# Kernel optimization log

Measured on AMD Instinct MI355X. Metric: run time of the kernel, lower is better.

Reference implementation:

```python
import jax, jax.numpy as jnp
import numpy as np

# Mamba2 config derived from __init__ defaults
D_MODEL, D_STATE, D_CONV, EXPAND, HEADDIM = 768, 16, 4, 2, 64
D_INNER = EXPAND * D_MODEL                      # 1536
NHEADS = D_INNER // HEADDIM                     # 24
NGROUPS = 1
CONV_DIM = D_INNER + 2 * NGROUPS * D_STATE      # 1568
D_IN_PROJ = 2 * D_INNER + 2 * NGROUPS * D_STATE + NHEADS  # 3128
EPS = 1e-5


def setup_inputs() -> dict:
    key = jax.random.key(0)
    ks = jax.random.split(key, 8)
    B, L = 2, 4096
    x = jax.random.normal(ks[0], (B, L, D_MODEL), jnp.float32)
    s_in = 1.0 / np.sqrt(D_MODEL)
    s_out = 1.0 / np.sqrt(D_INNER)
    W_in = jax.random.uniform(ks[1], (D_IN_PROJ, D_MODEL), jnp.float32, -s_in, s_in)
    W_out = jax.random.uniform(ks[2], (D_MODEL, D_INNER), jnp.float32, -s_out, s_out)
    conv_w = jax.random.uniform(ks[3], (CONV_DIM, D_CONV), jnp.float32, -0.5, 0.5)
    conv_b = jax.random.uniform(ks[4], (CONV_DIM,), jnp.float32, -0.5, 0.5)
    # dt init in [1e-3, 0.1] (log-uniform), stored as inverse-softplus bias
    dt = jnp.exp(jax.random.uniform(ks[5], (NHEADS,), jnp.float32) * (np.log(0.1) - np.log(1e-3)) + np.log(1e-3))
    dt_bias = dt + jnp.log(-jnp.expm1(-dt))
    A_log = jnp.log(jax.random.uniform(ks[6], (NHEADS,), jnp.float32, 1.0, 16.0))
    D = jnp.ones((NHEADS,), jnp.float32)
    ln_w = jnp.ones((D_MODEL,), jnp.float32)
    ln_b = jnp.zeros((D_MODEL,), jnp.float32)
    gate_norm_w = jnp.ones((D_INNER,), jnp.float32)
    return dict(x=x, ln_w=ln_w, ln_b=ln_b, W_in=W_in, conv_w=conv_w, conv_b=conv_b,
                dt_bias=dt_bias, A_log=A_log, D=D, gate_norm_w=gate_norm_w, W_out=W_out)


def _layernorm(x, w, b):
    mu = x.mean(-1, keepdims=True)
    var = ((x - mu) ** 2).mean(-1, keepdims=True)
    return (x - mu) * jax.lax.rsqrt(var + EPS) * w + b


def _silu(x):
    return x * jax.nn.sigmoid(x)


def _mamba_block(x, ln_w, ln_b, W_in, conv_w, conv_b, dt_bias, A_log, D, gate_norm_w, W_out):
    Bsz, L, _ = x.shape
    u = _layernorm(x, ln_w, ln_b)
    zxbcdt = jnp.einsum('bld,ed->ble', u, W_in)                 # (b,l,3128)
    z = zxbcdt[..., :D_INNER]
    xBC = zxbcdt[..., D_INNER:D_INNER + CONV_DIM]
    dt = jax.nn.softplus(zxbcdt[..., -NHEADS:] + dt_bias)       # (b,l,h)
    # causal depthwise conv (width D_CONV) + SiLU
    xp = jnp.pad(xBC, ((0, 0), (D_CONV - 1, 0), (0, 0)))
    acc = xp[:, 0:L, :] * conv_w[:, 0]
    for i in range(1, D_CONV):
        acc = acc + xp[:, i:i + L, :] * conv_w[:, i]
    xBC = _silu(acc + conv_b)
    xs = xBC[..., :D_INNER].reshape(Bsz, L, NHEADS, HEADDIM)    # (b,l,h,p)
    Bm = xBC[..., D_INNER:D_INNER + D_STATE]                    # (b,l,n) ngroups=1
    Cm = xBC[..., D_INNER + D_STATE:]                           # (b,l,n)
    A = -jnp.exp(A_log)                                         # (h,)
    dA = jnp.exp(dt * A)                                        # (b,l,h)
    # selective scan: h_t = dA_t * h_{t-1} + dt_t * (x_t outer B_t)
    def step(h, inp):
        dA_t, dt_t, B_t, C_t, x_t = inp                          # (b,h),(b,h),(b,n),(b,n),(b,h,p)
        h = dA_t[..., None, None] * h + jnp.einsum('bh,bn,bhp->bhpn', dt_t, B_t, x_t)
        y = jnp.einsum('bhpn,bn->bhp', h, C_t)
        return h, y
    h0 = jnp.zeros((Bsz, NHEADS, HEADDIM, D_STATE), x.dtype)
    _, ys = jax.lax.scan(step, h0, (dA.transpose(1, 0, 2), dt.transpose(1, 0, 2),
                                    Bm.transpose(1, 0, 2), Cm.transpose(1, 0, 2),
                                    xs.transpose(1, 0, 2, 3)))
    y = ys.transpose(1, 0, 2, 3) + D[:, None] * xs               # (b,l,h,p) skip term
    y = y.reshape(Bsz, L, D_INNER)
    # gated RMSNorm: norm(y * silu(z)) * weight
    g = y * _silu(z)
    g = g * jax.lax.rsqrt((g * g).mean(-1, keepdims=True) + EPS) * gate_norm_w
    out = jnp.einsum('ble,de->bld', g, W_out)
    return x + out


def reference(x, ln_w, ln_b, W_in, conv_w, conv_b, dt_bias, A_log, D, gate_norm_w, W_out):
    return _mamba_block(x, ln_w, ln_b, W_in, conv_w, conv_b, dt_bias, A_log, D, gate_norm_w, W_out)
```

## Files before the change

kernel.cpp:

```cpp
#include <hip/hip_runtime.h>
#include <hip/hip_bf16.h>
#include <stdint.h>

#define SEQ      4096
#define BATCH    2
#define NTOK     (BATCH*SEQ)
#define DMODEL   768
#define DINNER   1536
#define NHEADS   24
#define HEADDIM  64
#define DSTATE   16
#define NPAD     3200
#define EPSV     1e-5f
#define CHUNK    64
#define NCHUNK   (SEQ/CHUNK)
#define SUB      32
#define LNBLK    2048

typedef __bf16 bf16x8 __attribute__((ext_vector_type(8)));
typedef float  floatx4 __attribute__((ext_vector_type(4)));

__device__ __forceinline__ unsigned short f2bf(float f) {
    union { float f; uint32_t u; } v; v.f = f;
    uint32_t u = v.u;
    uint32_t r = (u + 0x7fffu + ((u >> 16) & 1u)) >> 16;
    return (unsigned short)r;
}

__device__ __forceinline__ float bf2f(unsigned short h) {
    union { uint32_t u; float f; } v; v.u = (uint32_t)h << 16;
    return v.f;
}

__device__ __forceinline__ float bfl(uint32_t u) {
    union { uint32_t u; float f; } v; v.u = u << 16; return v.f;
}
__device__ __forceinline__ float bfh(uint32_t u) {
    union { uint32_t u; float f; } v; v.u = u & 0xffff0000u; return v.f;
}
__device__ __forceinline__ uint32_t packbf(float lo, float hi) {
    return (uint32_t)f2bf(lo) | ((uint32_t)f2bf(hi) << 16);
}

__device__ __forceinline__ float siluf(float x) { return x / (1.f + __expf(-x)); }

__device__ __forceinline__ void async_cp16(const void* g, void* l) {
    __builtin_amdgcn_global_load_lds(
        (const __attribute__((address_space(1))) void*)g,
        (__attribute__((address_space(3))) void*)l,
        16, 0, 0);
}

__global__ __launch_bounds__(256) void prep_kernel(
    const float* __restrict__ x, const float* __restrict__ lnw, const float* __restrict__ lnb,
    unsigned short* __restrict__ u16,
    const float* __restrict__ Win, const float* __restrict__ Wout,
    const float* __restrict__ gw,
    unsigned short* __restrict__ win16, unsigned short* __restrict__ wout16)
{
    if (blockIdx.x < LNBLK) {
        int wave = threadIdx.x >> 6, lane = threadIdx.x & 63;
        int token = blockIdx.x * 4 + wave;
        const float* row = x + (size_t)token * DMODEL;
        float4 v[3];
        float s = 0.f, ss = 0.f;
#pragma unroll
        for (int j = 0; j < 3; ++j) {
            v[j] = *(const float4*)(row + lane*4 + j*256);
            s  += v[j].x + v[j].y + v[j].z + v[j].w;
            ss += v[j].x*v[j].x + v[j].y*v[j].y + v[j].z*v[j].z + v[j].w*v[j].w;
        }
#pragma unroll
        for (int o = 32; o > 0; o >>= 1) { s += __shfl_xor(s, o, 64); ss += __shfl_xor(ss, o, 64); }
        float mean = s * (1.f/768.f);
        float var  = ss * (1.f/768.f) - mean*mean;
        float rstd = rsqrtf(var + EPSV);
        unsigned short* brow = u16 + (size_t)token * DMODEL;
#pragma unroll
        for (int j = 0; j < 3; ++j) {
            int cidx = lane*4 + j*256;
            float4 w4 = *(const float4*)(lnw + cidx);
            float4 b4 = *(const float4*)(lnb + cidx);
            float a0 = (v[j].x - mean)*rstd*w4.x + b4.x;
            float a1 = (v[j].y - mean)*rstd*w4.y + b4.y;
            float a2 = (v[j].z - mean)*rstd*w4.z + b4.z;
            float a3 = (v[j].w - mean)*rstd*w4.w + b4.w;
            ushort4 p; p.x = f2bf(a0); p.y = f2bf(a1); p.z = f2bf(a2); p.w = f2bf(a3);
            *(ushort4*)(brow + cidx) = p;
        }
    } else {
        int e = ((blockIdx.x - LNBLK) * 256 + threadIdx.x) * 4;
        const int n1 = NPAD * DMODEL;
        if (e < n1) {
            int r = e / DMODEL;
            ushort4 p = {0, 0, 0, 0};
            if (r < 3128) {
                float4 v = *(const float4*)(Win + e);
                p.x = f2bf(v.x); p.y = f2bf(v.y); p.z = f2bf(v.z); p.w = f2bf(v.w);
            }
            *(ushort4*)(win16 + e) = p;
        } else {
            int e2 = e - n1;
            if (e2 < DMODEL * DINNER) {
                int row = e2 / DINNER;
                int col = e2 - row * DINNER;
                float4 v = *(const float4*)(Wout + e2);
                float4 w = *(const float4*)(gw + col);
                ushort4 p; p.x = f2bf(v.x*w.x); p.y = f2bf(v.y*w.y);
                           p.z = f2bf(v.z*w.z); p.w = f2bf(v.w*w.w);
                *(ushort4*)(wout16 + e2) = p;
            }
        }
    }
}

__global__ __launch_bounds__(256) void dt_kernel(
    const float* __restrict__ raw24, const float* __restrict__ dt_bias,
    const float* __restrict__ A_log, float* __restrict__ dtT, float* __restrict__ dAT)
{
    int tid = blockIdx.x * 256 + threadIdx.x;
    int h   = tid >> 13;
    int tok = tid & (NTOK-1);
    float raw = raw24[(size_t)tok*NHEADS + h] + dt_bias[h];
    float dt = (raw > 20.f) ? raw : log1pf(__expf(raw));
    float A = -__expf(A_log[h]);
    dtT[tid] = dt;
    dAT[tid] = __expf(dt * A);
}

__global__ __launch_bounds__(256, 3) void gemm1_kernel(
    const unsigned short* __restrict__ A, const unsigned short* __restrict__ Bt,
    unsigned short* __restrict__ z16, unsigned short* __restrict__ x16,
    float* __restrict__ bcr, float* __restrict__ raw24)
{
    constexpr int K = DMODEL;
    __shared__ unsigned short As[128*64];
    __shared__ unsigned short Bs[128*64];
    const int tid  = threadIdx.x;
    const int lane = tid & 63;
    const int wave = tid >> 6;
    const int id   = blockIdx.x;
    const int xcd  = id & 7;
    const int j5   = id >> 3;
    const int m0 = (xcd*8 + (j5 & 7)) * 128;
    const int n0 = (j5 >> 3) * 128;
    const int wm = (wave & 1) * 64;
    const int wn = (wave >> 1) * 64;

    floatx4 acc[4][4];
#pragma unroll
    for (int i = 0; i < 4; ++i)
#pragma unroll
        for (int j = 0; j < 4; ++j) acc[i][j] = floatx4{0.f, 0.f, 0.f, 0.f};

    const int srow8  = lane >> 3;
    const int schunk = lane & 7;
    const int sscol  = (schunk ^ srow8) * 8;

    for (int k0 = 0; k0 < K; k0 += 64) {
        __syncthreads();
#pragma unroll
        for (int o = 0; o < 4; ++o) {
            int row = wave*32 + o*8 + srow8;
            async_cp16(A + (size_t)(m0 + row) * K + k0 + sscol, As + row*64 + schunk*8);
        }
#pragma unroll
        for (int o = 0; o < 4; ++o) {
            int row = wave*32 + o*8 + srow8;
            async_cp16(Bt + (size_t)(n0 + row) * K + k0 + sscol, Bs + row*64 + schunk*8);
        }
        __syncthreads();
        const int fr  = lane & 15;
        const int q8  = lane >> 4;
        const int key = fr & 7;
#pragma unroll
        for (int ks = 0; ks < 2; ++ks) {
            const int ch = ((ks*4 + q8) ^ key) * 8;
            bf16x8 a[4], b[4];
#pragma unroll
            for (int i = 0; i < 4; ++i)
                a[i] = *(const bf16x8*)(As + (wm + i*16 + fr)*64 + ch);
#pragma unroll
            for (int j = 0; j < 4; ++j)
                b[j] = *(const bf16x8*)(Bs + (wn + j*16 + fr)*64 + ch);
#pragma unroll
            for (int i = 0; i < 4; ++i)
#pragma unroll
                for (int j = 0; j < 4; ++j)
                    acc[i][j] = __builtin_amdgcn_mfma_f32_16x16x32_bf16(a[i], b[j], acc[i][j], 0, 0, 0);
        }
    }

    const int col = lane & 15;
    const int rq  = (lane >> 4) * 4;
    if (n0 < DINNER) {
#pragma unroll
        for (int i = 0; i < 4; ++i)
#pragma unroll
            for (int j = 0; j < 4; ++j)
#pragma unroll
                for (int r = 0; r < 4; ++r) {
                    int gm = m0 + wm + i*16 + rq + r;
                    int gn = n0 + wn + j*16 + col;
                    z16[(size_t)gm * DINNER + gn] = f2bf(acc[i][j][r]);
                }
    } else if (n0 < 3072) {
#pragma unroll
        for (int i = 0; i < 4; ++i)
#pragma unroll
            for (int j = 0; j < 4; ++j)
#pragma unroll
                for (int r = 0; r < 4; ++r) {
                    int gm = m0 + wm + i*16 + rq + r;
                    int gn = n0 + wn + j*16 + col;
                    x16[(size_t)gm * DINNER + (gn - DINNER)] = f2bf(acc[i][j][r]);
                }
    } else {
#pragma unroll
        for (int i = 0; i < 4; ++i)
#pragma unroll
            for (int j = 0; j < 4; ++j)
#pragma unroll
                for (int r = 0; r < 4; ++r) {
                    int gm = m0 + wm + i*16 + rq + r;
                    int gn = n0 + wn + j*16 + col;
                    if (gn < 3104)
                        bcr[(size_t)gm * 32 + (gn - 3072)] = acc[i][j][r];
                    else if (gn < 3128)
                        raw24[(size_t)gm * NHEADS + (gn - 3104)] = acc[i][j][r];
                }
    }
}

__global__ __launch_bounds__(256, 4) void gemm2_kernel(
    const unsigned short* __restrict__ A, const unsigned short* __restrict__ Bt,
    float* __restrict__ Cf, const float* __restrict__ resid, const float* __restrict__ ssb)
{
    constexpr int K = DINNER;
    __shared__ unsigned short As[64*64];
    __shared__ unsigned short Bs[128*64];
    const int tid  = threadIdx.x;
    const int lane = tid & 63;
    const int wave = tid >> 6;
    const int id   = blockIdx.x;
    const int xcd  = id & 7;
    const int j6   = id >> 3;
    const int m0 = (xcd*16 + j6/6) * 64;
    const int n0 = (j6 % 6) * 128;
    const int wm = (wave & 1) * 32;
    const int wn = (wave >> 1) * 64;

    floatx4 acc[2][4];
#pragma unroll
    for (int i = 0; i < 2; ++i)
#pragma unroll
        for (int j = 0; j < 4; ++j) acc[i][j] = floatx4{0.f, 0.f, 0.f, 0.f};

    const int srow8  = lane >> 3;
    const int schunk = lane & 7;
    const int sscol  = (schunk ^ srow8) * 8;

    for (int k0 = 0; k0 < K; k0 += 64) {
        __syncthreads();
#pragma unroll
        for (int o = 0; o < 2; ++o) {
            int row = wave*16 + o*8 + srow8;
            async_cp16(A + (size_t)(m0 + row) * K + k0 + sscol, As + row*64 + schunk*8);
        }
#pragma unroll
        for (int o = 0; o < 4; ++o) {
            int row = wave*32 + o*8 + srow8;
            async_cp16(Bt + (size_t)(n0 + row) * K + k0 + sscol, Bs + row*64 + schunk*8);
        }
        __syncthreads();
        const int fr  = lane & 15;
        const int q8  = lane >> 4;
        const int key = fr & 7;
#pragma unroll
        for (int ks = 0; ks < 2; ++ks) {
            const int ch = ((ks*4 + q8) ^ key) * 8;
            bf16x8 a[2], b[4];
#pragma unroll
            for (int i = 0; i < 2; ++i)
                a[i] = *(const bf16x8*)(As + (wm + i*16 + fr)*64 + ch);
#pragma unroll
            for (int j = 0; j < 4; ++j)
                b[j] = *(const bf16x8*)(Bs + (wn + j*16 + fr)*64 + ch);
#pragma unroll
            for (int i = 0; i < 2; ++i)
#pragma unroll
                for (int j = 0; j < 4; ++j)
                    acc[i][j] = __builtin_amdgcn_mfma_f32_16x16x32_bf16(a[i], b[j], acc[i][j], 0, 0, 0);
        }
    }

    const int col = lane & 15;
    const int rq  = (lane >> 4) * 4;
#pragma unroll
    for (int i = 0; i < 2; ++i)
#pragma unroll
        for (int r = 0; r < 4; ++r) {
            int gm = m0 + wm + i*16 + rq + r;
            float sc = rsqrtf(ssb[gm] * (1.f/1536.f) + EPSV);
#pragma unroll
            for (int j = 0; j < 4; ++j) {
                int gn = n0 + wn + j*16 + col;
                Cf[(size_t)gm * DMODEL + gn] = acc[i][j][r] * sc + resid[(size_t)gm * DMODEL + gn];
            }
        }
}

__global__ __launch_bounds__(256) void scan_pass1(
    const unsigned short* __restrict__ x16, const float* __restrict__ bcr,
    const float* __restrict__ dAT, const float* __restrict__ dtT,
    const float* __restrict__ cw, const float* __restrict__ cb, const float* __restrict__ Dp,
    float* __restrict__ hloc, float* __restrict__ pprod, unsigned short* __restrict__ ylocal16)
{
    int wave = threadIdx.x >> 6, lane = threadIdx.x & 63;
    int blk = blockIdx.x * 4 + wave;
    int c = blk & (NCHUNK-1), bh = blk >> 6;
    int h = bh % NHEADS, b = bh / NHEADS;
    int row0 = b * SEQ + c * CHUNK;
    int l0 = c * CHUNK;
    int tb = h * NTOK + row0;
    __shared__ float bcraw[4][35][32];
    __shared__ float bcsc[4][32][32];
    __shared__ float av[4][32], dv[4][32];

    const int cx = h*64 + lane;
    float cwx0 = cw[cx*4+0], cwx1 = cw[cx*4+1], cwx2 = cw[cx*4+2], cwx3 = cw[cx*4+3];
    float cbx = cb[cx];
    const int nBC = lane & 31;
    float cwc0 = cw[(DINNER+nBC)*4+0], cwc1 = cw[(DINNER+nBC)*4+1];
    float cwc2 = cw[(DINNER+nBC)*4+2], cwc3 = cw[(DINNER+nBC)*4+3];
    float cbc = cb[DINNER+nBC];
    float Dh = Dp[h];

    float xm3 = (l0 >= 3) ? bf2f(x16[(size_t)(row0-3)*DINNER + cx]) : 0.f;
    float xm2 = (l0 >= 2) ? bf2f(x16[(size_t)(row0-2)*DINNER + cx]) : 0.f;
    float xm1 = (l0 >= 1) ? bf2f(x16[(size_t)(row0-1)*DINNER + cx]) : 0.f;

    float hst[16];
#pragma unroll
    for (int n = 0; n < 16; ++n) hst[n] = 0.f;
    float aprod = 1.f;

    for (int sc = 0; sc < CHUNK/SUB; ++sc) {
        int rb = row0 + sc * SUB;
        int lb = l0 + sc * SUB;
        __syncthreads();
#pragma unroll
        for (int it = 0; it < 5; ++it) {
            int idx = it*64 + lane;
            if (idx < 280) {
                int s = idx >> 3, q = idx & 7;
                float4 val = {0.f,0.f,0.f,0.f};
                if (lb - 3 + s >= 0)
                    val = *(const float4*)(bcr + (size_t)(rb-3+s)*32 + q*4);
                *(float4*)&bcraw[wave][s][q*4] = val;
            }
        }
        if (lane < 32) av[wave][lane] = dAT[(size_t)tb + sc*SUB + lane];
        else           dv[wave][lane-32] = dtT[(size_t)tb + sc*SUB + lane - 32];
        float xr[SUB];
#pragma unroll
        for (int s = 0; s < SUB; ++s)
            xr[s] = bf2f(x16[(size_t)(rb+s)*DINNER + cx]);
        __syncthreads();
#pragma unroll
        for (int it = 0; it < 16; ++it) {
            int s = it*2 + (lane >> 5);
            float v = cbc + bcraw[wave][s][nBC]*cwc0 + bcraw[wave][s+1][nBC]*cwc1
                          + bcraw[wave][s+2][nBC]*cwc2 + bcraw[wave][s+3][nBC]*cwc3;
            bcsc[wave][s][nBC] = siluf(v);
        }
        __syncthreads();
#pragma unroll 2
        for (int s = 0; s < SUB; ++s) {
            float a = av[wave][s];
            float xc = siluf(cbx + xm3*cwx0 + xm2*cwx1 + xm1*cwx2 + xr[s]*cwx3);
            xm3 = xm2; xm2 = xm1; xm1 = xr[s];
            float scale = dv[wave][s] * xc;
            float y = Dh * xc;
            const float4* bp4 = (const float4*)&bcsc[wave][s][0];
            float4 bv[8];
#pragma unroll
            for (int q = 0; q < 8; ++q) bv[q] = bp4[q];
            const float* bp = (const float*)bv;
#pragma unroll
            for (int n = 0; n < 16; ++n) hst[n] = a*hst[n] + scale*bp[n];
#pragma unroll
            for (int n = 0; n < 16; ++n) y += hst[n] * bp[16+n];
            aprod *= a;
            ylocal16[(size_t)(rb+s)*DINNER + cx] = f2bf(y);
        }
    }
    float* o = hloc + (size_t)blk * 1024 + lane * 16;
#pragma unroll
    for (int n = 0; n < 16; ++n) o[n] = hst[n];
    if (lane == 0) pprod[blk] = aprod;
}

__global__ __launch_bounds__(256) void scan_pass2(
    const float* __restrict__ hloc, const float* __restrict__ pprod,
    float* __restrict__ hstart, float* __restrict__ ssb)
{
    __shared__ float sm[64*256];
    __shared__ float pp[64];
    const int tid = threadIdx.x;
    const int bh  = blockIdx.x >> 2;
    const int q   = blockIdx.x & 3;
    int gt = blockIdx.x * 256 + tid;
    if (gt < NTOK) ssb[gt] = 0.f;
    const float* src = hloc + (size_t)bh * 65536 + q * 256;
#pragma unroll
    for (int it = 0; it < 16; ++it) {
        int idx = it*256 + tid;
        int c   = idx >> 6;
        int e4  = (idx & 63) * 4;
        *(float4*)&sm[c*256 + e4] = *(const float4*)(src + (size_t)c*1024 + e4);
    }
    if (tid < 64) pp[tid] = pprod[bh*64 + tid];
    __syncthreads();
    float h = 0.f;
    float* dst = hstart + (size_t)bh * 65536 + q * 256 + tid;
#pragma unroll 8
    for (int c = 0; c < 64; ++c) {
        dst[(size_t)c * 1024] = h;
        h = pp[c] * h + sm[c*256 + tid];
    }
}

__global__ __launch_bounds__(256) void scan_pass3(
    const float* __restrict__ bcr, const float* __restrict__ dAT,
    const float* __restrict__ cw, const float* __restrict__ cb,
    const float* __restrict__ hstart, const unsigned short* __restrict__ z16,
    unsigned short* __restrict__ ylocal16, float* __restrict__ ssb)
{
    int wave = threadIdx.x >> 6, lane = threadIdx.x & 63;
    int blk = blockIdx.x * 4 + wave;
    int c = blk & (NCHUNK-1), bh = blk >> 6;
    int h = bh % NHEADS, b = bh / NHEADS;
    int row0 = b * SEQ + c * CHUNK;
    int l0 = c * CHUNK;
    int tb = h * NTOK + row0;
    __shared__ float craw[4][35][16];
    __shared__ float csc[4][32][16];
    __shared__ float av[4][32];

    const int cx = h*64 + lane;
    const int nC = lane & 15;
    float cwc0 = cw[(DINNER+16+nC)*4+0], cwc1 = cw[(DINNER+16+nC)*4+1];
    float cwc2 = cw[(DINNER+16+nC)*4+2], cwc3 = cw[(DINNER+16+nC)*4+3];
    float cbc = cb[DINNER+16+nC];

    float h0[16];
    const float* hs = hstart + (size_t)blk * 1024 + lane * 16;
#pragma unroll
    for (int n = 0; n < 16; ++n) h0[n] = hs[n];
    float cd = 1.f;

    for (int sc = 0; sc < CHUNK/SUB; ++sc) {
        int rb = row0 + sc * SUB;
        int lb = l0 + sc * SUB;
        __syncthreads();
#pragma unroll
        for (int it = 0; it < 3; ++it) {
            int idx = it*64 + lane;
            if (idx < 140) {
                int s = idx >> 2, q = idx & 3;
                float4 val = {0.f,0.f,0.f,0.f};
                if (lb - 3 + s >= 0)
                    val = *(const float4*)(bcr + (size_t)(rb-3+s)*32 + 16 + q*4);
                *(float4*)&craw[wave][s][q*4] = val;
            }
        }
        if (lane < 32) av[wave][lane] = dAT[(size_t)tb + sc*SUB + lane];
        float yr[SUB], zr[SUB];
#pragma unroll
        for (int s = 0; s < SUB; ++s) {
            yr[s] = bf2f(ylocal16[(size_t)(rb+s)*DINNER + cx]);
            zr[s] = bf2f(z16[(size_t)(rb+s)*DINNER + cx]);
        }
        __syncthreads();
#pragma unroll
        for (int it = 0; it < 8; ++it) {
            int s = it*4 + (lane >> 4);
            float v = cbc + craw[wave][s][nC]*cwc0 + craw[wave][s+1][nC]*cwc1
                          + craw[wave][s+2][nC]*cwc2 + craw[wave][s+3][nC]*cwc3;
            csc[wave][s][nC] = siluf(v);
        }
        __syncthreads();
#pragma unroll 2
        for (int s = 0; s < SUB; ++s) {
            cd *= av[wave][s];
            const float4* cp4 = (const float4*)&csc[wave][s][0];
            float4 cv[4];
#pragma unroll
            for (int q = 0; q < 4; ++q) cv[q] = cp4[q];
            const float* cp = (const float*)cv;
            float corr = 0.f;
#pragma unroll
            for (int n = 0; n < 16; ++n) corr += cp[n] * h0[n];
            float g = (yr[s] + cd * corr) * siluf(zr[s]);
            float ssp = g * g;
#pragma unroll
            for (int o = 32; o > 0; o >>= 1) ssp += __shfl_xor(ssp, o, 64);
            if (lane == 0) atomicAdd(&ssb[rb + s], ssp);
            ylocal16[(size_t)(rb+s)*DINNER + cx] = f2bf(g);
        }
    }
}

extern "C" void kernel_launch(void* const* d_in, const int* in_sizes, int n_in,
                              void* d_out, int out_size, void* d_ws, size_t ws_size,
                              hipStream_t stream)
{
    const float* x        = (const float*)d_in[0];
    const float* ln_w     = (const float*)d_in[1];
    const float* ln_b     = (const float*)d_in[2];
    const float* W_in     = (const float*)d_in[3];
    const float* conv_w   = (const float*)d_in[4];
    const float* conv_b   = (const float*)d_in[5];
    const float* dt_bias  = (const float*)d_in[6];
    const float* A_log    = (const float*)d_in[7];
    const float* Dp       = (const float*)d_in[8];
    const float* gate_w   = (const float*)d_in[9];
    const float* W_out    = (const float*)d_in[10];
    float* out = (float*)d_out;

    char* ws = (char*)d_ws;
    size_t off = 0;
    auto alloc = [&](size_t bytes) -> void* {
        void* p = ws + off;
        off += (bytes + 255) & ~(size_t)255;
        return p;
    };
    unsigned short* u16    = (unsigned short*)alloc((size_t)NTOK*DMODEL*2);
    unsigned short* win16  = (unsigned short*)alloc((size_t)NPAD*DMODEL*2);
    float*          dtT    = (float*)alloc((size_t)NTOK*NHEADS*4);
    float*          dAT    = (float*)alloc((size_t)NTOK*NHEADS*4);
    float*          raw24  = (float*)alloc((size_t)NTOK*NHEADS*4);
    unsigned short* x16    = (unsigned short*)alloc((size_t)NTOK*DINNER*2);
    float*          bcr    = (float*)alloc((size_t)NTOK*32*4);
    unsigned short* wout16 = (unsigned short*)alloc((size_t)DMODEL*DINNER*2);
    unsigned short* z16    = (unsigned short*)alloc((size_t)NTOK*DINNER*2);
    unsigned short* y16    = (unsigned short*)alloc((size_t)NTOK*DINNER*2);
    unsigned short* g16    = (unsigned short*)alloc((size_t)NTOK*DINNER*2);
    float*          pprod  = (float*)alloc((size_t)BATCH*NHEADS*NCHUNK*4);
    float*          ssb    = (float*)alloc((size_t)NTOK*4);
    float* hloc   = (float*)u16;
    float* hstart = (float*)g16;

    prep_kernel<<<LNBLK + (NPAD*DMODEL + DMODEL*DINNER)/1024, 256, 0, stream>>>(
        x, ln_w, ln_b, u16, W_in, W_out, gate_w, win16, wout16);
    gemm1_kernel<<<1600, 256, 0, stream>>>(u16, win16, z16, x16, bcr, raw24);
    dt_kernel<<<NTOK*NHEADS/256, 256, 0, stream>>>(raw24, dt_bias, A_log, dtT, dAT);
    scan_pass1<<<BATCH*NHEADS*NCHUNK/4, 256, 0, stream>>>(x16, bcr, dAT, dtT, conv_w, conv_b, Dp, hloc, pprod, y16);
    scan_pass2<<<BATCH*NHEADS*4, 256, 0, stream>>>(hloc, pprod, hstart, ssb);
    scan_pass3<<<BATCH*NHEADS*NCHUNK/4, 256, 0, stream>>>(bcr, dAT, conv_w, conv_b, hstart, z16, y16, ssb);
    gemm2_kernel<<<768, 256, 0, stream>>>(y16, wout16, out, x, ssb);
}
```

Baseline: 271.9 us.

## Fuse dt computation into scan pass1 and RMS sum-of-squares into gemm2

Drops the separate dt_kernel: scan_pass1 now computes softplus(dt) and exp(dt*A) from raw24 directly and writes dAT for pass3, so the dtT buffer is no longer needed. The per-row sum of squares for the gated RMSNorm is also removed from scan_pass3, which used a wave reduction plus a global atomicAdd per row. gemm2 now computes it from the bf16 A tiles already staged in LDS on each k-step and keeps it in shared memory. This cuts a kernel launch, the atomics and the ssb zeroing, at the cost of some extra LDS reads and ALU work inside the GEMM loop. The norm is now taken over bf16-rounded values rather than fp32.

```diff
diff --git a/kernel.cpp b/kernel.cpp
--- a/kernel.cpp
+++ b/kernel.cpp
@@ -37,9 +37,6 @@
 }
 __device__ __forceinline__ float bfh(uint32_t u) {
     union { uint32_t u; float f; } v; v.u = u & 0xffff0000u; return v.f;
-}
-__device__ __forceinline__ uint32_t packbf(float lo, float hi) {
-    return (uint32_t)f2bf(lo) | ((uint32_t)f2bf(hi) << 16);
 }
 
 __device__ __forceinline__ float siluf(float x) { return x / (1.f + __expf(-x)); }
@@ -114,20 +111,6 @@
     }
 }
 
-__global__ __launch_bounds__(256) void dt_kernel(
-    const float* __restrict__ raw24, const float* __restrict__ dt_bias,
-    const float* __restrict__ A_log, float* __restrict__ dtT, float* __restrict__ dAT)
-{
-    int tid = blockIdx.x * 256 + threadIdx.x;
-    int h   = tid >> 13;
-    int tok = tid & (NTOK-1);
-    float raw = raw24[(size_t)tok*NHEADS + h] + dt_bias[h];
-    float dt = (raw > 20.f) ? raw : log1pf(__expf(raw));
-    float A = -__expf(A_log[h]);
-    dtT[tid] = dt;
-    dAT[tid] = __expf(dt * A);
-}
-
 __global__ __launch_bounds__(256, 3) void gemm1_kernel(
     const unsigned short* __restrict__ A, const unsigned short* __restrict__ Bt,
     unsigned short* __restrict__ z16, unsigned short* __restrict__ x16,
@@ -234,11 +217,12 @@
 
 __global__ __launch_bounds__(256, 4) void gemm2_kernel(
     const unsigned short* __restrict__ A, const unsigned short* __restrict__ Bt,
-    float* __restrict__ Cf, const float* __restrict__ resid, const float* __restrict__ ssb)
+    float* __restrict__ Cf, const float* __restrict__ resid)
 {
     constexpr int K = DINNER;
     __shared__ unsigned short As[64*64];
     __shared__ unsigned short Bs[128*64];
+    __shared__ float rowss[64];
     const int tid  = threadIdx.x;
     const int lane = tid & 63;
     const int wave = tid >> 6;
@@ -260,6 +244,10 @@
     const int schunk = lane & 7;
     const int sscol  = (schunk ^ srow8) * 8;
 
+    const int sr0 = tid >> 3;
+    const int scc = ((tid & 7) ^ (sr0 & 7)) * 8;
+    float rs0 = 0.f, rs1 = 0.f;
+
     for (int k0 = 0; k0 < K; k0 += 64) {
         __syncthreads();
 #pragma unroll
@@ -292,7 +280,22 @@
                 for (int j = 0; j < 4; ++j)
                     acc[i][j] = __builtin_amdgcn_mfma_f32_16x16x32_bf16(a[i], b[j], acc[i][j], 0, 0, 0);
         }
-    }
+        bf16x8 q0 = *(const bf16x8*)(As + sr0*64 + scc);
+        bf16x8 q1 = *(const bf16x8*)(As + (sr0 + 32)*64 + scc);
+#pragma unroll
+        for (int e = 0; e < 8; ++e) {
+            float f0 = (float)q0[e]; rs0 += f0*f0;
+            float f1 = (float)q1[e]; rs1 += f1*f1;
+        }
+    }
+
+    rs0 += __shfl_xor(rs0, 1, 64); rs0 += __shfl_xor(rs0, 2, 64); rs0 += __shfl_xor(rs0, 4, 64);
+    rs1 += __shfl_xor(rs1, 1, 64); rs1 += __shfl_xor(rs1, 2, 64); rs1 += __shfl_xor(rs1, 4, 64);
+    if ((lane & 7) == 0) {
+        rowss[wave*8 + (lane >> 3)]      = rs0;
+        rowss[wave*8 + 32 + (lane >> 3)] = rs1;
+    }
+    __syncthreads();
 
     const int col = lane & 15;
     const int rq  = (lane >> 4) * 4;
@@ -300,8 +303,9 @@
     for (int i = 0; i < 2; ++i)
 #pragma unroll
         for (int r = 0; r < 4; ++r) {
-            int gm = m0 + wm + i*16 + rq + r;
-            float sc = rsqrtf(ssb[gm] * (1.f/1536.f) + EPSV);
+            int lrow = wm + i*16 + rq + r;
+            int gm = m0 + lrow;
+            float sc = rsqrtf(rowss[lrow] * (1.f/1536.f) + EPSV);
 #pragma unroll
             for (int j = 0; j < 4; ++j) {
                 int gn = n0 + wn + j*16 + col;
@@ -312,9 +316,11 @@
 
 __global__ __launch_bounds__(256) void scan_pass1(
     const unsigned short* __restrict__ x16, const float* __restrict__ bcr,
-    const float* __restrict__ dAT, const float* __restrict__ dtT,
+    const float* __restrict__ raw24, const float* __restrict__ dt_bias,
+    const float* __restrict__ A_log,
     const float* __restrict__ cw, const float* __restrict__ cb, const float* __restrict__ Dp,
-    float* __restrict__ hloc, float* __restrict__ pprod, unsigned short* __restrict__ ylocal16)
+    float* __restrict__ hloc, float* __restrict__ pprod,
+    unsigned short* __restrict__ ylocal16, float* __restrict__ dAT)
 {
     int wave = threadIdx.x >> 6, lane = threadIdx.x & 63;
     int blk = blockIdx.x * 4 + wave;
@@ -335,6 +341,8 @@
     float cwc2 = cw[(DINNER+nBC)*4+2], cwc3 = cw[(DINNER+nBC)*4+3];
     float cbc = cb[DINNER+nBC];
     float Dh = Dp[h];
+    float dtb = dt_bias[h];
+    float Ah  = -__expf(A_log[h]);
 
     float xm3 = (l0 >= 3) ? bf2f(x16[(size_t)(row0-3)*DINNER + cx]) : 0.f;
     float xm2 = (l0 >= 2) ? bf2f(x16[(size_t)(row0-2)*DINNER + cx]) : 0.f;
@@ -360,8 +368,14 @@
                 *(float4*)&bcraw[wave][s][q*4] = val;
             }
         }
-        if (lane < 32) av[wave][lane] = dAT[(size_t)tb + sc*SUB + lane];
-        else           dv[wave][lane-32] = dtT[(size_t)tb + sc*SUB + lane - 32];
+        if (lane < 32) {
+            float raw = raw24[(size_t)(rb + lane)*NHEADS + h] + dtb;
+            float dt = (raw > 20.f) ? raw : log1pf(__expf(raw));
+            float dA = __expf(dt * Ah);
+            av[wave][lane] = dA;
+            dv[wave][lane] = dt;
+            dAT[(size_t)tb + sc*SUB + lane] = dA;
+        }
         float xr[SUB];
 #pragma unroll
         for (int s = 0; s < SUB; ++s)
@@ -402,16 +416,13 @@
 }
 
 __global__ __launch_bounds__(256) void scan_pass2(
-    const float* __restrict__ hloc, const float* __restrict__ pprod,
-    float* __restrict__ hstart, float* __restrict__ ssb)
+    const float* __restrict__ hloc, const float* __restrict__ pprod, float* __restrict__ hstart)
 {
     __shared__ float sm[64*256];
     __shared__ float pp[64];
     const int tid = threadIdx.x;
     const int bh  = blockIdx.x >> 2;
     const int q   = blockIdx.x & 3;
-    int gt = blockIdx.x * 256 + tid;
-    if (gt < NTOK) ssb[gt] = 0.f;
     const float* src = hloc + (size_t)bh * 65536 + q * 256;
 #pragma unroll
     for (int it = 0; it < 16; ++it) {
@@ -435,7 +446,7 @@
     const float* __restrict__ bcr, const float* __restrict__ dAT,
     const float* __restrict__ cw, const float* __restrict__ cb,
     const float* __restrict__ hstart, const unsigned short* __restrict__ z16,
-    unsigned short* __restrict__ ylocal16, float* __restrict__ ssb)
+    unsigned short* __restrict__ ylocal16)
 {
     int wave = threadIdx.x >> 6, lane = threadIdx.x & 63;
     int blk = blockIdx.x * 4 + wave;
@@ -503,10 +514,6 @@
 #pragma unroll
             for (int n = 0; n < 16; ++n) corr += cp[n] * h0[n];
             float g = (yr[s] + cd * corr) * siluf(zr[s]);
-            float ssp = g * g;
-#pragma unroll
-            for (int o = 32; o > 0; o >>= 1) ssp += __shfl_xor(ssp, o, 64);
-            if (lane == 0) atomicAdd(&ssb[rb + s], ssp);
             ylocal16[(size_t)(rb+s)*DINNER + cx] = f2bf(g);
         }
     }
@@ -538,7 +545,6 @@
     };
     unsigned short* u16    = (unsigned short*)alloc((size_t)NTOK*DMODEL*2);
     unsigned short* win16  = (unsigned short*)alloc((size_t)NPAD*DMODEL*2);
-    float*          dtT    = (float*)alloc((size_t)NTOK*NHEADS*4);
     float*          dAT    = (float*)alloc((size_t)NTOK*NHEADS*4);
     float*          raw24  = (float*)alloc((size_t)NTOK*NHEADS*4);
     unsigned short* x16    = (unsigned short*)alloc((size_t)NTOK*DINNER*2);
@@ -548,16 +554,15 @@
     unsigned short* y16    = (unsigned short*)alloc((size_t)NTOK*DINNER*2);
     unsigned short* g16    = (unsigned short*)alloc((size_t)NTOK*DINNER*2);
     float*          pprod  = (float*)alloc((size_t)BATCH*NHEADS*NCHUNK*4);
-    float*          ssb    = (float*)alloc((size_t)NTOK*4);
     float* hloc   = (float*)u16;
     float* hstart = (float*)g16;
 
     prep_kernel<<<LNBLK + (NPAD*DMODEL + DMODEL*DINNER)/1024, 256, 0, stream>>>(
         x, ln_w, ln_b, u16, W_in, W_out, gate_w, win16, wout16);
     gemm1_kernel<<<1600, 256, 0, stream>>>(u16, win16, z16, x16, bcr, raw24);
-    dt_kernel<<<NTOK*NHEADS/256, 256, 0, stream>>>(raw24, dt_bias, A_log, dtT, dAT);
-    scan_pass1<<<BATCH*NHEADS*NCHUNK/4, 256, 0, stream>>>(x16, bcr, dAT, dtT, conv_w, conv_b, Dp, hloc, pprod, y16);
-    scan_pass2<<<BATCH*NHEADS*4, 256, 0, stream>>>(hloc, pprod, hstart, ssb);
-    scan_pass3<<<BATCH*NHEADS*NCHUNK/4, 256, 0, stream>>>(bcr, dAT, conv_w, conv_b, hstart, z16, y16, ssb);
-    gemm2_kernel<<<768, 256, 0, stream>>>(y16, wout16, out, x, ssb);
-}
+    scan_pass1<<<BATCH*NHEADS*NCHUNK/4, 256, 0, stream>>>(
+        x16, bcr, raw24, dt_bias, A_log, conv_w, conv_b, Dp, hloc, pprod, y16, dAT);
+    scan_pass2<<<BATCH*NHEADS*4, 256, 0, stream>>>(hloc, pprod, hstart);
+    scan_pass3<<<BATCH*NHEADS*NCHUNK/4, 256, 0, stream>>>(bcr, dAT, conv_w, conv_b, hstart, z16, y16);
+    gemm2_kernel<<<768, 256, 0, stream>>>(y16, wout16, out, x);
+}
```

Measured after the change: 251.7 us. -7.4%, faster.
